# Performance work log

Measured on AMD Instinct MI355X. Metric: run time of the kernel, lower is better.

Reference implementation:

```python
import jax, jax.numpy as jnp
import numpy as np


def setup_inputs() -> dict:
    key = jax.random.key(0)
    k1, k2, k3, k4 = jax.random.split(key, 4)
    B, Q, K, H, D = 2, 2048, 2048, 16, 128
    qs = jax.random.normal(k1, (B, Q, H, D), dtype=jnp.float32)
    ks = jax.random.normal(k2, (B, K, H, D), dtype=jnp.float32)
    vs = jax.random.normal(k3, (B, K, H, D), dtype=jnp.float32)
    valid_lens = jax.random.randint(k4, (B,), 1, K + 1, dtype=jnp.int32)
    return {"qs": qs, "ks": ks, "vs": vs, "valid_lens": valid_lens}


def reference(qs, ks, vs, valid_lens):
    B, Q, H, D = qs.shape
    K = ks.shape[1]
    # rearrange 'B L H D -> (B H) L D'
    q = qs.transpose(0, 2, 1, 3).reshape(B * H, Q, D)
    k = ks.transpose(0, 2, 1, 3).reshape(B * H, K, D)
    v = vs.transpose(0, 2, 1, 3).reshape(B * H, K, D)
    # DotScorer: scaled dot product -> (B*H, Q, K)
    scores = jnp.einsum('bqd,bkd->bqk', q, k) / jnp.sqrt(jnp.float32(D))
    # mask_attn: key positions >= valid_len get large negative score
    vl = jnp.repeat(valid_lens, H)                         # (B*H,)
    mask = jnp.arange(K)[None, None, :] < vl[:, None, None]
    scores = jnp.where(mask, scores, jnp.float32(-1e6))
    attn = jax.nn.softmax(scores, axis=-1)
    # dropout is identity (p_dropout=0 / not training)
    ctx = attn @ v                                         # (B*H, Q, D)
    ctx = ctx.reshape(B, H, Q, D).transpose(0, 2, 1, 3)    # (B, Q, H, D)
    return ctx, attn.reshape(B, H, Q, K)
```

## Files before the change

### kernel.cpp

```cpp
#include <hip/hip_runtime.h>
#include <hip/hip_bf16.h>
#include <stdint.h>

#define B_ 2
#define Qn 2048
#define Kn 2048
#define Hn 16
#define Dn 128
#define QT 256
#define KT 128
#define HD (Hn*Dn)
#define KROW 132
#define VROW 136

typedef __bf16 bf16x8 __attribute__((ext_vector_type(8)));
typedef __bf16 bf16x4 __attribute__((ext_vector_type(4)));
typedef float f32x4 __attribute__((ext_vector_type(4)));
typedef float f32x16 __attribute__((ext_vector_type(16)));

union BF8 { __bf16 e[8]; bf16x8 v; };

#define SCALE 0.088388347648318447f

struct SMs {
  unsigned short K[2][KT][KROW];
  unsigned short V[2][Dn][VROW];
};

__device__ __forceinline__ void bar_lgkm() {
  asm volatile("s_waitcnt lgkmcnt(0)" ::: "memory");
  __builtin_amdgcn_s_barrier();
  __builtin_amdgcn_sched_barrier(0);
}

__device__ __forceinline__ bf16x4 cvt4(f32x4 a) {
  bf16x4 r;
  r[0] = (__bf16)a[0]; r[1] = (__bf16)a[1];
  r[2] = (__bf16)a[2]; r[3] = (__bf16)a[3];
  return r;
}

__device__ __forceinline__ void stage_k(const float* kb, unsigned short (*dst)[KROW], int tid) {
  #pragma unroll
  for (int ii = 0; ii < 8; ++ii) {
    int chunk = ii * 512 + tid;
    int row = chunk >> 5, cv = chunk & 31;
    f32x4 a = *(const f32x4*)(kb + (size_t)row * HD + cv * 4);
    *(bf16x4*)&dst[row][cv * 4] = cvt4(a);
  }
}

__device__ __forceinline__ void stage_v(const float* vb, unsigned short (*dst)[VROW], int tid) {
  int d = tid & 127, c0 = tid >> 7;
  const float* colp = vb + d;
  #pragma unroll
  for (int rr = 0; rr < 4; ++rr) {
    int idx = rr * 4 + c0;
    int base = (idx >> 2) * 32 + ((idx >> 1) & 1) * 16 + (idx & 1) * 4;
    BF8 t;
    #pragma unroll
    for (int j = 0; j < 4; ++j) {
      t.e[j]     = (__bf16)colp[(size_t)(base + j) * HD];
      t.e[4 + j] = (__bf16)colp[(size_t)(base + 8 + j) * HD];
    }
    *(bf16x8*)&dst[d][idx * 8] = t.v;
  }
}

__global__ __launch_bounds__(512, 2) void attn_fwd(
    const float* __restrict__ qs, const float* __restrict__ ks,
    const float* __restrict__ vs, const int* __restrict__ vlen,
    float* __restrict__ ctx_out, float* __restrict__ attn_out)
{
  __shared__ __align__(16) SMs sm;

  const int tid = threadIdx.x, wave = tid >> 6, lane = tid & 63;
  const int l31 = lane & 31, hi = lane >> 5;

  const int L   = blockIdx.x;
  const int xcd = L & 7;
  const int i5  = L >> 3;
  const int bh  = ((i5 & 3) << 3) + xcd;
  const int qt  = i5 >> 2;
  const int b   = bh >> 4, h = bh & 15;
  const int vl  = vlen[b];
  const int qbw = qt * QT + wave * 32;

  BF8 qf[8];
  {
    const float* qrow = qs + (((size_t)(b * Qn + qbw + l31)) * Hn + h) * Dn;
    #pragma unroll
    for (int s = 0; s < 8; ++s) {
      int d0 = s * 16 + hi * 8;
      f32x4 a0 = *(const f32x4*)(qrow + d0);
      f32x4 a1 = *(const f32x4*)(qrow + d0 + 4);
      #pragma unroll
      for (int j = 0; j < 4; ++j) { qf[s].e[j] = (__bf16)a0[j]; qf[s].e[4 + j] = (__bf16)a1[j]; }
    }
  }

  const float* kbase = ks + ((size_t)b * Kn * Hn + h) * Dn;
  const float* vbase = vs + ((size_t)b * Kn * Hn + h) * Dn;
  const int nkt = (vl + KT - 1) / KT;

  float rs = 0.f;
  stage_k(kbase, sm.K[0], tid);
  bar_lgkm();
  for (int t = 0; t < nkt; ++t) {
    const int cur = t & 1;
    if (t + 1 < nkt) stage_k(kbase + (size_t)(t + 1) * KT * HD, sm.K[cur ^ 1], tid);
    #pragma unroll
    for (int m = 0; m < 4; ++m) {
      f32x16 acc;
      #pragma unroll
      for (int i = 0; i < 16; ++i) acc[i] = 0.f;
      #pragma unroll
      for (int s = 0; s < 8; ++s) {
        BF8 kf; kf.v = *(const bf16x8*)&sm.K[cur][m * 32 + l31][s * 16 + hi * 8];
        acc = __builtin_amdgcn_mfma_f32_32x32x16_bf16(kf.v, qf[s].v, acc, 0, 0, 0);
      }
      const int kb0 = t * KT + m * 32 + hi * 4;
      #pragma unroll
      for (int reg = 0; reg < 16; ++reg) {
        int key = kb0 + (reg & 3) + 8 * (reg >> 2);
        rs += (key < vl) ? __expf(acc[reg] * SCALE) : 0.f;
      }
    }
    bar_lgkm();
  }
  rs += __shfl_xor(rs, 32);
  const float inv = 1.0f / rs;

  f32x16 ctxa[4];
  #pragma unroll
  for (int ch = 0; ch < 4; ++ch)
    #pragma unroll
    for (int i = 0; i < 16; ++i) ctxa[ch][i] = 0.f;

  stage_k(kbase, sm.K[0], tid);
  stage_v(vbase, sm.V[0], tid);
  bar_lgkm();
  float* rowp = attn_out + ((size_t)bh * Qn + qbw + l31) * Kn;
  for (int t = 0; t < nkt; ++t) {
    const int cur = t & 1;
    if (t + 1 < nkt) {
      stage_k(kbase + (size_t)(t + 1) * KT * HD, sm.K[cur ^ 1], tid);
      stage_v(vbase + (size_t)(t + 1) * KT * HD, sm.V[cur ^ 1], tid);
    }
    #pragma unroll
    for (int m = 0; m < 4; ++m) {
      f32x16 acc;
      #pragma unroll
      for (int i = 0; i < 16; ++i) acc[i] = 0.f;
      #pragma unroll
      for (int s = 0; s < 8; ++s) {
        BF8 kf; kf.v = *(const bf16x8*)&sm.K[cur][m * 32 + l31][s * 16 + hi * 8];
        acc = __builtin_amdgcn_mfma_f32_32x32x16_bf16(kf.v, qf[s].v, acc, 0, 0, 0);
      }
      const int kb0 = t * KT + m * 32;
      BF8 pf0, pf1;
      #pragma unroll
      for (int r4 = 0; r4 < 4; ++r4) {
        f32x4 p;
        #pragma unroll
        for (int rr = 0; rr < 4; ++rr) {
          int key = kb0 + r4 * 8 + hi * 4 + rr;
          float v = (key < vl) ? __expf(acc[r4 * 4 + rr] * SCALE) * inv : 0.f;
          p[rr] = v;
          if (r4 < 2) pf0.e[r4 * 4 + rr] = (__bf16)v;
          else        pf1.e[(r4 - 2) * 4 + rr] = (__bf16)v;
        }
        *(f32x4*)(rowp + kb0 + r4 * 8 + hi * 4) = p;
      }
      #pragma unroll
      for (int ch = 0; ch < 4; ++ch) {
        BF8 v0; v0.v = *(const bf16x8*)&sm.V[cur][ch * 32 + l31][(m * 4 + hi) * 8];
        ctxa[ch] = __builtin_amdgcn_mfma_f32_32x32x16_bf16(v0.v, pf0.v, ctxa[ch], 0, 0, 0);
        BF8 v1; v1.v = *(const bf16x8*)&sm.V[cur][ch * 32 + l31][(m * 4 + 2 + hi) * 8];
        ctxa[ch] = __builtin_amdgcn_mfma_f32_32x32x16_bf16(v1.v, pf1.v, ctxa[ch], 0, 0, 0);
      }
    }
    bar_lgkm();
  }

  const int col0 = nkt * KT;
  #pragma unroll 1
  for (int r = 0; r < 32; ++r) {
    float* zp = attn_out + ((size_t)bh * Qn + qbw + r) * Kn;
    for (int c4 = col0 + lane * 4; c4 < Kn; c4 += 256)
      *(f32x4*)(zp + c4) = (f32x4){0.f, 0.f, 0.f, 0.f};
  }

  float* cp = ctx_out + (((size_t)(b * Qn + qbw + l31)) * Hn + h) * Dn;
  #pragma unroll
  for (int ch = 0; ch < 4; ++ch)
    #pragma unroll
    for (int r4 = 0; r4 < 4; ++r4) {
      f32x4 o;
      #pragma unroll
      for (int rr = 0; rr < 4; ++rr) o[rr] = ctxa[ch][r4 * 4 + rr];
      *(f32x4*)(cp + ch * 32 + r4 * 8 + hi * 4) = o;
    }
}

extern "C" void kernel_launch(void* const* d_in, const int* in_sizes, int n_in,
                              void* d_out, int out_size, void* d_ws, size_t ws_size,
                              hipStream_t stream) {
  const float* qs   = (const float*)d_in[0];
  const float* ks   = (const float*)d_in[1];
  const float* vs   = (const float*)d_in[2];
  const int*   vlen = (const int*)d_in[3];
  float* ctx  = (float*)d_out;
  float* attn = ctx + (size_t)B_ * Qn * Hn * Dn;
  attn_fwd<<<dim3((Qn / QT) * B_ * Hn), 512, 0, stream>>>(qs, ks, vs, vlen, ctx, attn);
}
```

Measured before the change: 215.6 us.

## Shrink Q tile and split K tile sizes per pass with masking only on boundary tile

Halves the query tile to 128 rows with 256 threads (doubling block count), keeps a 128-key tile for the row-sum pass but uses 64-key K/V tiles in the output pass, sharing shared memory through a union. Key masking is applied only on the final partial tile, and the row sums use four partial accumulators to break the dependency chain. The aim is more blocks for occupancy and load balance and less per-element compare work, at the cost of re-staging K/V more often per query row and smaller tiles per barrier.

After: 228.8 us. 6.1% more time.

```diff
diff --git a/kernel.cpp b/kernel.cpp
--- a/kernel.cpp
+++ b/kernel.cpp
@@ -7,11 +7,12 @@
 #define Kn 2048
 #define Hn 16
 #define Dn 128
-#define QT 256
-#define KT 128
+#define QT 128
+#define KT 64
+#define KT1 128
 #define HD (Hn*Dn)
 #define KROW 132
-#define VROW 136
+#define VROW 72
 
 typedef __bf16 bf16x8 __attribute__((ext_vector_type(8)));
 typedef __bf16 bf16x4 __attribute__((ext_vector_type(4)));
@@ -22,10 +23,8 @@
 
 #define SCALE 0.088388347648318447f
 
-struct SMs {
-  unsigned short K[2][KT][KROW];
-  unsigned short V[2][Dn][VROW];
-};
+struct SMp2 { unsigned short K[2][KT][KROW]; unsigned short V[2][Dn][VROW]; };
+union SMu { SMp2 p2; unsigned short K1[2][KT1][KROW]; };
 
 __device__ __forceinline__ void bar_lgkm() {
   asm volatile("s_waitcnt lgkmcnt(0)" ::: "memory");
@@ -40,22 +39,32 @@
   return r;
 }
 
-__device__ __forceinline__ void stage_k(const float* kb, unsigned short (*dst)[KROW], int tid) {
+__device__ __forceinline__ void stage_k64(const float* kb, unsigned short (*dst)[KROW], int tid) {
   #pragma unroll
   for (int ii = 0; ii < 8; ++ii) {
-    int chunk = ii * 512 + tid;
+    int chunk = ii * 256 + tid;
     int row = chunk >> 5, cv = chunk & 31;
     f32x4 a = *(const f32x4*)(kb + (size_t)row * HD + cv * 4);
     *(bf16x4*)&dst[row][cv * 4] = cvt4(a);
   }
 }
 
-__device__ __forceinline__ void stage_v(const float* vb, unsigned short (*dst)[VROW], int tid) {
-  int d = tid & 127, c0 = tid >> 7;
+__device__ __forceinline__ void stage_k128(const float* kb, unsigned short (*dst)[KROW], int tid) {
+  #pragma unroll
+  for (int ii = 0; ii < 16; ++ii) {
+    int chunk = ii * 256 + tid;
+    int row = chunk >> 5, cv = chunk & 31;
+    f32x4 a = *(const f32x4*)(kb + (size_t)row * HD + cv * 4);
+    *(bf16x4*)&dst[row][cv * 4] = cvt4(a);
+  }
+}
+
+__device__ __forceinline__ void stage_v64(const float* vb, unsigned short (*dst)[VROW], int tid) {
+  int d = tid & 127, t0 = tid >> 7;
   const float* colp = vb + d;
   #pragma unroll
   for (int rr = 0; rr < 4; ++rr) {
-    int idx = rr * 4 + c0;
+    int idx = rr * 2 + t0;
     int base = (idx >> 2) * 32 + ((idx >> 1) & 1) * 16 + (idx & 1) * 4;
     BF8 t;
     #pragma unroll
@@ -67,12 +76,12 @@
   }
 }
 
-__global__ __launch_bounds__(512, 2) void attn_fwd(
+__global__ __launch_bounds__(256, 2) void attn_fwd(
     const float* __restrict__ qs, const float* __restrict__ ks,
     const float* __restrict__ vs, const int* __restrict__ vlen,
     float* __restrict__ ctx_out, float* __restrict__ attn_out)
 {
-  __shared__ __align__(16) SMs sm;
+  __shared__ __align__(16) SMu sm;
 
   const int tid = threadIdx.x, wave = tid >> 6, lane = tid & 63;
   const int l31 = lane & 31, hi = lane >> 5;
@@ -101,33 +110,43 @@
 
   const float* kbase = ks + ((size_t)b * Kn * Hn + h) * Dn;
   const float* vbase = vs + ((size_t)b * Kn * Hn + h) * Dn;
-  const int nkt = (vl + KT - 1) / KT;
-
-  float rs = 0.f;
-  stage_k(kbase, sm.K[0], tid);
-  bar_lgkm();
-  for (int t = 0; t < nkt; ++t) {
-    const int cur = t & 1;
-    if (t + 1 < nkt) stage_k(kbase + (size_t)(t + 1) * KT * HD, sm.K[cur ^ 1], tid);
-    #pragma unroll
-    for (int m = 0; m < 4; ++m) {
-      f32x16 acc;
-      #pragma unroll
-      for (int i = 0; i < 16; ++i) acc[i] = 0.f;
-      #pragma unroll
-      for (int s = 0; s < 8; ++s) {
-        BF8 kf; kf.v = *(const bf16x8*)&sm.K[cur][m * 32 + l31][s * 16 + hi * 8];
-        acc = __builtin_amdgcn_mfma_f32_32x32x16_bf16(kf.v, qf[s].v, acc, 0, 0, 0);
-      }
-      const int kb0 = t * KT + m * 32 + hi * 4;
-      #pragma unroll
-      for (int reg = 0; reg < 16; ++reg) {
-        int key = kb0 + (reg & 3) + 8 * (reg >> 2);
-        rs += (key < vl) ? __expf(acc[reg] * SCALE) : 0.f;
-      }
-    }
+
+  f32x4 rsv = {0.f, 0.f, 0.f, 0.f};
+  {
+    const int nkt1 = (vl + KT1 - 1) / KT1;
+    const bool hasb1 = (vl & (KT1 - 1)) != 0;
+    stage_k128(kbase, sm.K1[0], tid);
     bar_lgkm();
-  }
+    for (int t = 0; t < nkt1; ++t) {
+      const int cur = t & 1;
+      if (t + 1 < nkt1) stage_k128(kbase + (size_t)(t + 1) * KT1 * HD, sm.K1[cur ^ 1], tid);
+      const bool mb = hasb1 && (t == nkt1 - 1);
+      #pragma unroll
+      for (int m = 0; m < 4; ++m) {
+        f32x16 acc;
+        #pragma unroll
+        for (int i = 0; i < 16; ++i) acc[i] = 0.f;
+        #pragma unroll
+        for (int s = 0; s < 8; ++s) {
+          BF8 kf; kf.v = *(const bf16x8*)&sm.K1[cur][m * 32 + l31][s * 16 + hi * 8];
+          acc = __builtin_amdgcn_mfma_f32_32x32x16_bf16(kf.v, qf[s].v, acc, 0, 0, 0);
+        }
+        if (!mb) {
+          #pragma unroll
+          for (int reg = 0; reg < 16; ++reg) rsv[reg & 3] += __expf(acc[reg] * SCALE);
+        } else {
+          const int kb0 = t * KT1 + m * 32 + hi * 4;
+          #pragma unroll
+          for (int reg = 0; reg < 16; ++reg) {
+            int key = kb0 + (reg & 3) + 8 * (reg >> 2);
+            rsv[reg & 3] += (key < vl) ? __expf(acc[reg] * SCALE) : 0.f;
+          }
+        }
+      }
+      bar_lgkm();
+    }
+  }
+  float rs = (rsv[0] + rsv[1]) + (rsv[2] + rsv[3]);
   rs += __shfl_xor(rs, 32);
   const float inv = 1.0f / rs;
 
@@ -137,24 +156,27 @@
     #pragma unroll
     for (int i = 0; i < 16; ++i) ctxa[ch][i] = 0.f;
 
-  stage_k(kbase, sm.K[0], tid);
-  stage_v(vbase, sm.V[0], tid);
+  const int nkt = (vl + KT - 1) / KT;
+  const bool hasb2 = (vl & (KT - 1)) != 0;
+  stage_k64(kbase, sm.p2.K[0], tid);
+  stage_v64(vbase, sm.p2.V[0], tid);
   bar_lgkm();
   float* rowp = attn_out + ((size_t)bh * Qn + qbw + l31) * Kn;
   for (int t = 0; t < nkt; ++t) {
     const int cur = t & 1;
     if (t + 1 < nkt) {
-      stage_k(kbase + (size_t)(t + 1) * KT * HD, sm.K[cur ^ 1], tid);
-      stage_v(vbase + (size_t)(t + 1) * KT * HD, sm.V[cur ^ 1], tid);
-    }
-    #pragma unroll
-    for (int m = 0; m < 4; ++m) {
+      stage_k64(kbase + (size_t)(t + 1) * KT * HD, sm.p2.K[cur ^ 1], tid);
+      stage_v64(vbase + (size_t)(t + 1) * KT * HD, sm.p2.V[cur ^ 1], tid);
+    }
+    const bool mb = hasb2 && (t == nkt - 1);
+    #pragma unroll
+    for (int m = 0; m < 2; ++m) {
       f32x16 acc;
       #pragma unroll
       for (int i = 0; i < 16; ++i) acc[i] = 0.f;
       #pragma unroll
       for (int s = 0; s < 8; ++s) {
-        BF8 kf; kf.v = *(const bf16x8*)&sm.K[cur][m * 32 + l31][s * 16 + hi * 8];
+        BF8 kf; kf.v = *(const bf16x8*)&sm.p2.K[cur][m * 32 + l31][s * 16 + hi * 8];
         acc = __builtin_amdgcn_mfma_f32_32x32x16_bf16(kf.v, qf[s].v, acc, 0, 0, 0);
       }
       const int kb0 = t * KT + m * 32;
@@ -162,21 +184,28 @@
       #pragma unroll
       for (int r4 = 0; r4 < 4; ++r4) {
         f32x4 p;
+        if (!mb) {
+          #pragma unroll
+          for (int rr = 0; rr < 4; ++rr) p[rr] = __expf(acc[r4 * 4 + rr] * SCALE) * inv;
+        } else {
+          #pragma unroll
+          for (int rr = 0; rr < 4; ++rr) {
+            int key = kb0 + r4 * 8 + hi * 4 + rr;
+            p[rr] = (key < vl) ? __expf(acc[r4 * 4 + rr] * SCALE) * inv : 0.f;
+          }
+        }
         #pragma unroll
         for (int rr = 0; rr < 4; ++rr) {
-          int key = kb0 + r4 * 8 + hi * 4 + rr;
-          float v = (key < vl) ? __expf(acc[r4 * 4 + rr] * SCALE) * inv : 0.f;
-          p[rr] = v;
-          if (r4 < 2) pf0.e[r4 * 4 + rr] = (__bf16)v;
-          else        pf1.e[(r4 - 2) * 4 + rr] = (__bf16)v;
+          if (r4 < 2) pf0.e[r4 * 4 + rr] = (__bf16)p[rr];
+          else        pf1.e[(r4 - 2) * 4 + rr] = (__bf16)p[rr];
         }
         *(f32x4*)(rowp + kb0 + r4 * 8 + hi * 4) = p;
       }
       #pragma unroll
       for (int ch = 0; ch < 4; ++ch) {
-        BF8 v0; v0.v = *(const bf16x8*)&sm.V[cur][ch * 32 + l31][(m * 4 + hi) * 8];
+        BF8 v0; v0.v = *(const bf16x8*)&sm.p2.V[cur][ch * 32 + l31][(m * 4 + hi) * 8];
         ctxa[ch] = __builtin_amdgcn_mfma_f32_32x32x16_bf16(v0.v, pf0.v, ctxa[ch], 0, 0, 0);
-        BF8 v1; v1.v = *(const bf16x8*)&sm.V[cur][ch * 32 + l31][(m * 4 + 2 + hi) * 8];
+        BF8 v1; v1.v = *(const bf16x8*)&sm.p2.V[cur][ch * 32 + l31][(m * 4 + 2 + hi) * 8];
         ctxa[ch] = __builtin_amdgcn_mfma_f32_32x32x16_bf16(v1.v, pf1.v, ctxa[ch], 0, 0, 0);
       }
     }
@@ -212,5 +241,5 @@
   const int*   vlen = (const int*)d_in[3];
   float* ctx  = (float*)d_out;
   float* attn = ctx + (size_t)B_ * Qn * Hn * Dn;
-  attn_fwd<<<dim3((Qn / QT) * B_ * Hn), 512, 0, stream>>>(qs, ks, vs, vlen, ctx, attn);
-}
+  attn_fwd<<<dim3((Qn / QT) * B_ * Hn), 256, 0, stream>>>(qs, ks, vs, vlen, ctx, attn);
+}
```
